# Kernel tuning notes

Measured on AMD Instinct MI355X. Metric: run time of the kernel, lower is better.

## Reference

```python
import jax, jax.numpy as jnp
import numpy as np

# Instant-NGP style multi-resolution hash grid (torch-ngp convention)
NUM_LEVELS = 32
LEVEL_DIM = 2
LOG2_T = 19
T = 1 << LOG2_T            # per-level hash table size (power of two)
BASE_RES = 1
PER_LEVEL_SCALE = 2.0
PRIMES = (1, 2654435761, 805459861)  # spatial hash primes (uint32, wraps)
# 8 corner offsets of the unit cube, [8, 3]
OFFSETS_NP = np.array([[(c >> d) & 1 for d in range(3)] for c in range(8)], dtype=np.uint32)


def hash_encode(x, embeddings):
    """x: [N,3] in [0,1); embeddings: [L, T, F] -> [N, L*F]."""
    offsets = jnp.asarray(OFFSETS_NP)                       # [8,3] uint32
    offs_f = offsets.astype(x.dtype)                        # [8,3]
    feats = []
    for l in range(NUM_LEVELS):
        scale = float(np.exp2(l * np.log2(PER_LEVEL_SCALE)) * BASE_RES - 1.0)
        res = int(np.ceil(scale)) + 1
        pos = x * jnp.float32(scale) + 0.5                  # [N,3]
        pos0 = jnp.floor(pos)
        frac = pos - pos0                                   # [N,3] in [0,1)
        pg = pos0.astype(jnp.uint32)                        # [N,3]
        corners = pg[:, None, :] + offsets[None, :, :]      # [N,8,3] uint32
        if res ** 3 <= T:
            # dense (non-colliding) linear index at coarse levels
            r = jnp.uint32(res)
            idx = corners[..., 0] + corners[..., 1] * r + corners[..., 2] * (r * r)
        else:
            # spatial hash: xor of coordinate * prime (uint32 wraparound)
            idx = (corners[..., 0] * jnp.uint32(PRIMES[0])
                   ^ corners[..., 1] * jnp.uint32(PRIMES[1])
                   ^ corners[..., 2] * jnp.uint32(PRIMES[2]))
        idx = (idx & jnp.uint32(T - 1)).astype(jnp.int32)   # [N,8]
        f = embeddings[l][idx]                              # gather -> [N,8,F]
        # trilinear interpolation weights
        w = jnp.prod(jnp.where(offs_f[None] == 1, frac[:, None, :], 1.0 - frac[:, None, :]), axis=-1)  # [N,8]
        feats.append(jnp.sum(f * w[..., None], axis=1))     # [N,F]
    return jnp.concatenate(feats, axis=-1)                  # [N, L*F]


def setup_inputs() -> dict:
    key = jax.random.key(0)
    k = jax.random.split(key, 5)
    N = 1 << 20
    x = jax.random.uniform(k[0], (N, 3), dtype=jnp.float32)
    embeddings = jax.random.normal(k[1], (NUM_LEVELS, T, LEVEL_DIM), dtype=jnp.float32) * 1e-2
    in_dim = NUM_LEVELS * LEVEL_DIM  # 64
    W1 = jax.random.normal(k[2], (in_dim, 128), dtype=jnp.float32) * (1.0 / np.sqrt(in_dim))
    b1 = jnp.zeros((128,), jnp.float32)
    W2 = jax.random.normal(k[3], (128, 128), dtype=jnp.float32) * (1.0 / np.sqrt(128))
    b2 = jnp.zeros((128,), jnp.float32)
    W3 = jax.random.normal(k[4], (128, 1), dtype=jnp.float32) * (1.0 / np.sqrt(128))
    b3 = jnp.zeros((1,), jnp.float32)
    return {"x": x, "embeddings": embeddings, "W1": W1, "b1": b1, "W2": W2, "b2": b2, "W3": W3, "b3": b3}


def reference(x, embeddings, W1, b1, W2, b2, W3, b3):
    h = hash_encode(x, embeddings)                 # [N, 64]
    h = jax.nn.relu(h @ W1 + b1)                   # [N, 128]
    h = jax.nn.relu(h @ W2 + b2)                   # [N, 128]
    return h @ W3 + b3                             # [N, 1]
```

## Files before the change

### kernel.cpp

```cpp
#include <hip/hip_runtime.h>
#include <stdint.h>


#define NLV 32
#define LOG2T 19
#define TSZ (1u << LOG2T)
#define TMASK (TSZ - 1u)
#define PRIME2 2654435761u
#define PRIME3 805459861u
#define NHASH 24

typedef float v2f __attribute__((ext_vector_type(2)));
typedef float f32x4 __attribute__((ext_vector_type(4)));
typedef float f32x4u __attribute__((ext_vector_type(4), aligned(8)));
typedef short bf16x8 __attribute__((ext_vector_type(8)));
typedef uint32_t u32x4 __attribute__((ext_vector_type(4)));

__device__ __forceinline__ uint32_t pack_bf16(float a, float b) {
  uint32_t ua = __float_as_uint(a), ub = __float_as_uint(b);
  ua = (ua + 0x7fffu + ((ua >> 16) & 1u)) >> 16;
  ub = (ub + 0x7fffu + ((ub >> 16) & 1u)) >> 16;
  return ua | (ub << 16);
}
__device__ __forceinline__ uint16_t bf16_rne(float a) {
  uint32_t u = __float_as_uint(a);
  u = (u + 0x7fffu + ((u >> 16) & 1u)) >> 16;
  return (uint16_t)u;
}

__device__ __forceinline__ uint32_t encode_level(
    float scale, uint32_t r, bool dense, const v2f* __restrict__ embl,
    float xv, float yv, float zv)
{
  float px = __fadd_rn(__fmul_rn(xv, scale), 0.5f);
  float py = __fadd_rn(__fmul_rn(yv, scale), 0.5f);
  float pz = __fadd_rn(__fmul_rn(zv, scale), 0.5f);
  float bx = floorf(px), by = floorf(py), bz = floorf(pz);
  float fx = __fsub_rn(px, bx), fy = __fsub_rn(py, by), fz = __fsub_rn(pz, bz);
  uint32_t gx = (uint32_t)bx, gy = (uint32_t)by, gz = (uint32_t)bz;
  float wx0 = __fsub_rn(1.0f, fx), wx1 = fx;
  float wy0 = __fsub_rn(1.0f, fy), wy1 = fy;
  float wz0 = __fsub_rn(1.0f, fz), wz1 = fz;
  const uint32_t rr = r * r;

  float f0 = 0.0f, f1 = 0.0f;
  #pragma unroll
  for (int cp = 0; cp < 4; ++cp) {
    uint32_t cy = gy + (uint32_t)(cp & 1);
    uint32_t cz = gz + (uint32_t)(cp >> 1);
    float wyz = __fmul_rn((cp & 1) ? wy1 : wy0, (cp >> 1) ? wz1 : wz0);
    v2f e0, e1;
    if (dense) {
      uint32_t i0 = gx + cy * r + cz * rr;
      f32x4 e2 = *(const f32x4u*)&embl[i0];
      e0[0] = e2.x; e0[1] = e2.y; e1[0] = e2.z; e1[1] = e2.w;
    } else {
      uint32_t h = (cy * PRIME2) ^ (cz * PRIME3);
      uint32_t i0 = (gx ^ h) & TMASK;
      if (!(gx & 1u)) {
        f32x4 e2 = *(const f32x4*)&embl[i0 & ~1u];
        bool odd = (i0 & 1u) != 0u;
        e0[0] = odd ? e2.z : e2.x; e0[1] = odd ? e2.w : e2.y;
        e1[0] = odd ? e2.x : e2.z; e1[1] = odd ? e2.y : e2.w;
      } else {
        uint32_t i1 = ((gx + 1u) ^ h) & TMASK;
        e0 = embl[i0];
        e1 = embl[i1];
      }
    }
    float w0 = __fmul_rn(wx0, wyz), w1 = __fmul_rn(wx1, wyz);
    f0 = fmaf(w0, e0[0], f0); f1 = fmaf(w0, e0[1], f1);
    f0 = fmaf(w1, e1[0], f0); f1 = fmaf(w1, e1[1], f1);
  }
  return pack_bf16(f0, f1);
}

__global__ __launch_bounds__(256) void encode_kernel(
    const float* __restrict__ x, const float* __restrict__ emb,
    uint32_t* __restrict__ feats, int offset, int count, int chunkCap, int bpl)
{
  const int bid = (int)blockIdx.x;
  const int xcd = bid & 7;
  const int j = bid >> 3;
  const int phase = j / bpl;
  const int within = j - phase * bpl;
  const int l = 7 + xcd + (phase << 3);

  const float scale = (float)((double)(1ULL << l) - 1.0);
  const v2f* __restrict__ embl = (const v2f*)(emb + ((size_t)l << (LOG2T + 1)));

  #pragma unroll
  for (int k = 0; k < 4; ++k) {
    int li = within * 1024 + k * 256 + (int)threadIdx.x;
    if (li < count) {
      int p = offset + li;
      float xv = __builtin_nontemporal_load(&x[3 * p + 0]);
      float yv = __builtin_nontemporal_load(&x[3 * p + 1]);
      float zv = __builtin_nontemporal_load(&x[3 * p + 2]);
      uint32_t f = encode_level(scale, 0u, false, embl, xv, yv, zv);
      __builtin_nontemporal_store(f, &feats[(size_t)(l - 7) * chunkCap + li]);
    }
  }
}

__global__ __launch_bounds__(512) void prep_kernel(
    const float* __restrict__ W1, const float* __restrict__ W2,
    uint16_t* __restrict__ wimg)
{
  int i = (int)blockIdx.x * 512 + (int)threadIdx.x;
  if (i < 8192) {
    int k = i >> 7, n = i & 127;
    wimg[(n * 128 + ((k * 2) ^ ((n & 7) << 4))) >> 1] = bf16_rne(W1[i]);
  } else if (i < 24576) {
    int t = i - 8192;
    int k = t >> 7, n = t & 127;
    wimg[(16384 + n * 256 + ((k * 2) ^ ((n & 7) << 4))) >> 1] = bf16_rne(W2[t]);
  }
}

#define MLP_G 64

__global__ __launch_bounds__(256, 2) void mlp_kernel(
    const float* __restrict__ x, const float* __restrict__ emb,
    const uint32_t* __restrict__ feats, const uint16_t* __restrict__ wimg,
    const float* __restrict__ b1, const float* __restrict__ b2,
    const float* __restrict__ W3, const float* __restrict__ b3,
    float* __restrict__ out, int offset, int count, int chunkCap, int nGroups)
{
  __shared__ char lds[65536];
  char* xh  = lds;
  char* wt1 = lds + 16384;
  char* wb  = lds + 32768;

  const int tid = (int)threadIdx.x;
  const int lane = tid & 63;
  const int w = tid >> 6;
  const int col = lane & 15;
  const int kh = lane >> 4;

  #pragma unroll
  for (int jj = 0; jj < 12; ++jj) {
    int i = tid + jj * 256;
    ((u32x4*)wt1)[i] = ((const u32x4*)wimg)[i];
  }

  const int pp = w * 16 + col;
  float bias1[8], bias2[8], w3v[8];
  #pragma unroll
  for (int nt = 0; nt < 8; ++nt) {
    int n = nt * 16 + col;
    bias1[nt] = b1[n]; bias2[nt] = b2[n]; w3v[nt] = W3[n];
  }
  const float b3v = b3[0];

  const int sp = tid & 63;
  const int sq = tid >> 6;

  for (int g = (int)blockIdx.x; g < nGroups; g += (int)gridDim.x) {
    const int base = g * MLP_G;
    __syncthreads();

    {
      int gp = base + sp;
      int src = (gp < count) ? gp : 0;
      u32x4 v0, v1;
      if (sq == 0) {
        float xv = x[3 * src + 0], yv = x[3 * src + 1], zv = x[3 * src + 2];
        uint32_t f[7];
        #pragma unroll
        for (int l = 0; l < 7; ++l) {
          const float scale = (float)((double)(1ULL << l) - 1.0);
          const v2f* embl = (const v2f*)(emb + ((size_t)l << (LOG2T + 1)));
          f[l] = encode_level(scale, 1u << l, true, embl, xv, yv, zv);
        }
        v0.x = f[0]; v0.y = f[1]; v0.z = f[2]; v0.w = f[3];
        v1.x = f[4]; v1.y = f[5]; v1.z = f[6];
        v1.w = __builtin_nontemporal_load(&feats[(size_t)0 * chunkCap + src]);
      } else if (sq == 3) {
        float xv = x[3 * src + 0], yv = x[3 * src + 1], zv = x[3 * src + 2];
        v0.x = __builtin_nontemporal_load(&feats[(size_t)17 * chunkCap + src]);
        v0.y = __builtin_nontemporal_load(&feats[(size_t)18 * chunkCap + src]);
        v0.z = __builtin_nontemporal_load(&feats[(size_t)19 * chunkCap + src]);
        v0.w = __builtin_nontemporal_load(&feats[(size_t)20 * chunkCap + src]);
        v1.x = __builtin_nontemporal_load(&feats[(size_t)21 * chunkCap + src]);
        v1.y = __builtin_nontemporal_load(&feats[(size_t)22 * chunkCap + src]);
        v1.z = __builtin_nontemporal_load(&feats[(size_t)23 * chunkCap + src]);
        const float s31 = (float)((double)(1ULL << 31) - 1.0);
        const v2f* embl = (const v2f*)(emb + ((size_t)31 << (LOG2T + 1)));
        v1.w = encode_level(s31, 0u, false, embl, xv, yv, zv);
      } else {
        int ib = sq * 8 - 7;
        v0.x = __builtin_nontemporal_load(&feats[(size_t)(ib + 0) * chunkCap + src]);
        v0.y = __builtin_nontemporal_load(&feats[(size_t)(ib + 1) * chunkCap + src]);
        v0.z = __builtin_nontemporal_load(&feats[(size_t)(ib + 2) * chunkCap + src]);
        v0.w = __builtin_nontemporal_load(&feats[(size_t)(ib + 3) * chunkCap + src]);
        v1.x = __builtin_nontemporal_load(&feats[(size_t)(ib + 4) * chunkCap + src]);
        v1.y = __builtin_nontemporal_load(&feats[(size_t)(ib + 5) * chunkCap + src]);
        v1.z = __builtin_nontemporal_load(&feats[(size_t)(ib + 6) * chunkCap + src]);
        v1.w = __builtin_nontemporal_load(&feats[(size_t)(ib + 7) * chunkCap + src]);
      }
      int sw = (sp & 7) << 4;
      *(u32x4*)(xh + sp * 256 + ((sq * 32 +  0) ^ sw)) = v0;
      *(u32x4*)(xh + sp * 256 + ((sq * 32 + 16) ^ sw)) = v1;
    }
    __syncthreads();

    f32x4 acc[8];
    #pragma unroll
    for (int nt = 0; nt < 8; ++nt) acc[nt] = {0.f, 0.f, 0.f, 0.f};
    #pragma unroll
    for (int kt = 0; kt < 2; ++kt) {
      bf16x8 a = *(const bf16x8*)(xh + pp * 256 + ((kt * 64 + kh * 16) ^ ((pp & 7) << 4)));
      #pragma unroll
      for (int nt = 0; nt < 8; ++nt) {
        int n = nt * 16 + col;
        bf16x8 b = *(const bf16x8*)(wt1 + n * 128 + ((kt * 64 + kh * 16) ^ ((n & 7) << 4)));
        acc[nt] = __builtin_amdgcn_mfma_f32_16x16x32_bf16(a, b, acc[nt], 0, 0, 0);
      }
    }

    #pragma unroll
    for (int nt = 0; nt < 8; ++nt) {
      int n = nt * 16 + col;
      #pragma unroll
      for (int rg = 0; rg < 4; ++rg) {
        int pr = w * 16 + kh * 4 + rg;
        float h = fmaxf(acc[nt][rg] + bias1[nt], 0.0f);
        *(uint16_t*)(xh + pr * 256 + ((n * 2) ^ ((pr & 7) << 4))) = bf16_rne(h);
      }
    }

    f32x4 acc2[8];
    #pragma unroll
    for (int nt = 0; nt < 8; ++nt) acc2[nt] = {0.f, 0.f, 0.f, 0.f};
    #pragma unroll
    for (int q = 0; q < 4; ++q) {
      bf16x8 a = *(const bf16x8*)(xh + pp * 256 + ((q * 64 + kh * 16) ^ ((pp & 7) << 4)));
      #pragma unroll
      for (int nt = 0; nt < 8; ++nt) {
        int n = nt * 16 + col;
        bf16x8 b = *(const bf16x8*)(wb + n * 256 + ((q * 64 + kh * 16) ^ ((n & 7) << 4)));
        acc2[nt] = __builtin_amdgcn_mfma_f32_16x16x32_bf16(a, b, acc2[nt], 0, 0, 0);
      }
    }

    float osum[4] = {0.f, 0.f, 0.f, 0.f};
    #pragma unroll
    for (int nt = 0; nt < 8; ++nt) {
      #pragma unroll
      for (int rg = 0; rg < 4; ++rg)
        osum[rg] = fmaf(fmaxf(acc2[nt][rg] + bias2[nt], 0.0f), w3v[nt], osum[rg]);
    }
    #pragma unroll
    for (int rg = 0; rg < 4; ++rg) {
      osum[rg] += __shfl_xor(osum[rg], 1);
      osum[rg] += __shfl_xor(osum[rg], 2);
      osum[rg] += __shfl_xor(osum[rg], 4);
      osum[rg] += __shfl_xor(osum[rg], 8);
    }
    #pragma unroll
    for (int rg = 0; rg < 4; ++rg) {
      if (col == rg) {
        int pr = base + w * 16 + kh * 4 + rg;
        if (pr < count) out[offset + pr] = osum[rg] + b3v;
      }
    }
  }
}

extern "C" void kernel_launch(void* const* d_in, const int* in_sizes, int n_in,
                              void* d_out, int out_size, void* d_ws, size_t ws_size,
                              hipStream_t stream) {
  const float* x   = (const float*)d_in[0];
  const float* emb = (const float*)d_in[1];
  const float* W1  = (const float*)d_in[2];
  const float* b1  = (const float*)d_in[3];
  const float* W2  = (const float*)d_in[4];
  const float* b2  = (const float*)d_in[5];
  const float* W3  = (const float*)d_in[6];
  const float* b3  = (const float*)d_in[7];
  float* out = (float*)d_out;
  const int N = in_sizes[0] / 3;

  uint16_t* wimg = (uint16_t*)d_ws;
  uint32_t* feats = (uint32_t*)((char*)d_ws + 49152);
  const size_t perPoint = (size_t)NHASH * sizeof(uint32_t);
  size_t avail = (ws_size > 49152) ? ws_size - 49152 : 0;
  size_t capz = avail / perPoint;
  if (capz > (size_t)N) capz = (size_t)N;
  int cap = (int)capz & ~1023;
  if (cap <= 0) cap = (N < 1024) ? N : 1024;

  prep_kernel<<<48, 512, 0, stream>>>(W1, W2, wimg);

  for (int off = 0; off < N; off += cap) {
    int cnt = (N - off < cap) ? (N - off) : cap;
    int bpl = (cnt + 1023) / 1024;
    encode_kernel<<<NHASH * bpl, 256, 0, stream>>>(x, emb, feats, off, cnt, cap, bpl);
    int nGroups = (cnt + MLP_G - 1) / MLP_G;
    int nb = nGroups < 2048 ? nGroups : 2048;
    mlp_kernel<<<nb, 256, 0, stream>>>(
        x, emb, feats, wimg, b1, b2, W3, b3, out, off, cnt, cap, nGroups);
  }
}
```

Before: 937.3 us.

## Balance per-lane level encoding and make staging wave-local to drop block barriers

```diff
diff --git a/kernel.cpp b/kernel.cpp
--- a/kernel.cpp
+++ b/kernel.cpp
@@ -15,6 +15,12 @@
 typedef float f32x4u __attribute__((ext_vector_type(4), aligned(8)));
 typedef short bf16x8 __attribute__((ext_vector_type(8)));
 typedef uint32_t u32x4 __attribute__((ext_vector_type(4)));
+
+__constant__ int Lmap[32] = {
+  0, 31,  7,  8,  9, 10, 11, 12,
+  1,  6, 13, 14, 15, 16, 17, 18,
+  2,  5, 19, 20, 21, 22, 23, 24,
+  3,  4, 25, 26, 27, 28, 29, 30};
 
 __device__ __forceinline__ uint32_t pack_bf16(float a, float b) {
   uint32_t ua = __float_as_uint(a), ub = __float_as_uint(b);
@@ -110,7 +116,8 @@
   int i = (int)blockIdx.x * 512 + (int)threadIdx.x;
   if (i < 8192) {
     int k = i >> 7, n = i & 127;
-    wimg[(n * 128 + ((k * 2) ^ ((n & 7) << 4))) >> 1] = bf16_rne(W1[i]);
+    int ok = 2 * Lmap[k >> 1] + (k & 1);
+    wimg[(n * 128 + ((k * 2) ^ ((n & 7) << 4))) >> 1] = bf16_rne(W1[ok * 128 + n]);
   } else if (i < 24576) {
     int t = i - 8192;
     int k = t >> 7, n = t & 127;
@@ -143,6 +150,7 @@
     int i = tid + jj * 256;
     ((u32x4*)wt1)[i] = ((const u32x4*)wimg)[i];
   }
+  __syncthreads();
 
   const int pp = w * 16 + col;
   float bias1[8], bias2[8], w3v[8];
@@ -153,57 +161,40 @@
   }
   const float b3v = b3[0];
 
-  const int sp = tid & 63;
-  const int sq = tid >> 6;
+  const int lp = lane & 15;
+  const int qq = lane >> 4;
+  const int srow = w * 16 + lp;
+  const int ssw = (srow & 7) << 4;
 
   for (int g = (int)blockIdx.x; g < nGroups; g += (int)gridDim.x) {
     const int base = g * MLP_G;
-    __syncthreads();
 
     {
-      int gp = base + sp;
+      int gp = base + srow;
       int src = (gp < count) ? gp : 0;
+      float xv = x[3 * src + 0], yv = x[3 * src + 1], zv = x[3 * src + 2];
+      uint32_t f[8];
+      {
+        float scale = (float)((1u << qq) - 1u);
+        const v2f* embl = (const v2f*)(emb + ((size_t)qq << (LOG2T + 1)));
+        f[0] = encode_level(scale, 1u << qq, true, embl, xv, yv, zv);
+      }
+      {
+        int lB = (qq == 0) ? 31 : (7 - qq);
+        float scale = (float)((1u << lB) - 1u);
+        const v2f* embl = (const v2f*)(emb + ((size_t)lB << (LOG2T + 1)));
+        f[1] = encode_level(scale, 1u << lB, qq != 0, embl, xv, yv, zv);
+      }
+      int fb = qq * 6;
+      #pragma unroll
+      for (int j = 0; j < 6; ++j)
+        f[2 + j] = __builtin_nontemporal_load(&feats[(size_t)(fb + j) * chunkCap + src]);
       u32x4 v0, v1;
-      if (sq == 0) {
-        float xv = x[3 * src + 0], yv = x[3 * src + 1], zv = x[3 * src + 2];
-        uint32_t f[7];
-        #pragma unroll
-        for (int l = 0; l < 7; ++l) {
-          const float scale = (float)((double)(1ULL << l) - 1.0);
-          const v2f* embl = (const v2f*)(emb + ((size_t)l << (LOG2T + 1)));
-          f[l] = encode_level(scale, 1u << l, true, embl, xv, yv, zv);
-        }
-        v0.x = f[0]; v0.y = f[1]; v0.z = f[2]; v0.w = f[3];
-        v1.x = f[4]; v1.y = f[5]; v1.z = f[6];
-        v1.w = __builtin_nontemporal_load(&feats[(size_t)0 * chunkCap + src]);
-      } else if (sq == 3) {
-        float xv = x[3 * src + 0], yv = x[3 * src + 1], zv = x[3 * src + 2];
-        v0.x = __builtin_nontemporal_load(&feats[(size_t)17 * chunkCap + src]);
-        v0.y = __builtin_nontemporal_load(&feats[(size_t)18 * chunkCap + src]);
-        v0.z = __builtin_nontemporal_load(&feats[(size_t)19 * chunkCap + src]);
-        v0.w = __builtin_nontemporal_load(&feats[(size_t)20 * chunkCap + src]);
-        v1.x = __builtin_nontemporal_load(&feats[(size_t)21 * chunkCap + src]);
-        v1.y = __builtin_nontemporal_load(&feats[(size_t)22 * chunkCap + src]);
-        v1.z = __builtin_nontemporal_load(&feats[(size_t)23 * chunkCap + src]);
-        const float s31 = (float)((double)(1ULL << 31) - 1.0);
-        const v2f* embl = (const v2f*)(emb + ((size_t)31 << (LOG2T + 1)));
-        v1.w = encode_level(s31, 0u, false, embl, xv, yv, zv);
-      } else {
-        int ib = sq * 8 - 7;
-        v0.x = __builtin_nontemporal_load(&feats[(size_t)(ib + 0) * chunkCap + src]);
-        v0.y = __builtin_nontemporal_load(&feats[(size_t)(ib + 1) * chunkCap + src]);
-        v0.z = __builtin_nontemporal_load(&feats[(size_t)(ib + 2) * chunkCap + src]);
-        v0.w = __builtin_nontemporal_load(&feats[(size_t)(ib + 3) * chunkCap + src]);
-        v1.x = __builtin_nontemporal_load(&feats[(size_t)(ib + 4) * chunkCap + src]);
-        v1.y = __builtin_nontemporal_load(&feats[(size_t)(ib + 5) * chunkCap + src]);
-        v1.z = __builtin_nontemporal_load(&feats[(size_t)(ib + 6) * chunkCap + src]);
-        v1.w = __builtin_nontemporal_load(&feats[(size_t)(ib + 7) * chunkCap + src]);
-      }
-      int sw = (sp & 7) << 4;
-      *(u32x4*)(xh + sp * 256 + ((sq * 32 +  0) ^ sw)) = v0;
-      *(u32x4*)(xh + sp * 256 + ((sq * 32 + 16) ^ sw)) = v1;
-    }
-    __syncthreads();
+      v0.x = f[0]; v0.y = f[1]; v0.z = f[2]; v0.w = f[3];
+      v1.x = f[4]; v1.y = f[5]; v1.z = f[6]; v1.w = f[7];
+      *(u32x4*)(xh + srow * 256 + ((qq * 32 +  0) ^ ssw)) = v0;
+      *(u32x4*)(xh + srow * 256 + ((qq * 32 + 16) ^ ssw)) = v1;
+    }
 
     f32x4 acc[8];
     #pragma unroll
```

Result: slower. 957.0 us (+2.1%).
